# Performance work log

Hardware: AMD Instinct MI355X
Metric: run time of the kernel (lower is better)

The kernel has to match this reference:

```python
import jax, jax.numpy as jnp
import numpy as np
from jax import lax

V = 30000   # vocab (input_types)
D = 512     # model_dim
H = D // 2  # per-direction LSTM hidden
R = 64      # relation_types
B = 32      # batch
T = 512     # seq len
E = 64      # max entities
L = 2       # lstm layers


def setup_inputs() -> dict:
    key = jax.random.key(0)
    ks = jax.random.split(key, 12)
    s = 0.02
    sents = jax.random.randint(ks[0], (B, T), 0, V, dtype=jnp.int64)
    # ent_inds[b, k] = (ent_id, start, end); -1 sentinel marks padding
    ids = np.tile(np.arange(E), (B, 1))
    starts = ids * 8
    ends = starts + 4  # 4-token spans, max end = 63*8+4 = 508 <= T
    ent = np.stack([ids, starts, ends], axis=-1).astype(np.int64)
    for b in range(1, B, 2):
        ent[b, E - 8:] = -1  # ragged: odd batches have 56 entities
    ent_inds = jnp.asarray(ent)
    emb = jax.random.normal(ks[1], (V, D), jnp.float32) * s
    Wih = jax.random.normal(ks[2], (L, 2, 4 * H, D), jnp.float32) * s
    Whh = jax.random.normal(ks[3], (L, 2, 4 * H, H), jnp.float32) * s
    bih = jnp.zeros((L, 2, 4 * H), jnp.float32)
    bhh = jnp.zeros((L, 2, 4 * H), jnp.float32)
    ln_g = jnp.ones((D,), jnp.float32)
    ln_b = jnp.zeros((D,), jnp.float32)
    rel1_w = jax.random.normal(ks[4], (D, D), jnp.float32) * s
    rel1_b = jnp.zeros((D,), jnp.float32)
    rel2_w = jax.random.normal(ks[5], (D, D), jnp.float32) * s
    rel2_b = jnp.zeros((D,), jnp.float32)
    proj_w = jax.random.normal(ks[6], (D, D), jnp.float32) * s
    proj_b = jnp.zeros((D,), jnp.float32)
    dec_w = jax.random.normal(ks[7], (R, D), jnp.float32) * s
    dec_b = jnp.zeros((R,), jnp.float32)
    return dict(sents=sents, ent_inds=ent_inds, max_ents=E, emb=emb,
                Wih=Wih, Whh=Whh, bih=bih, bhh=bhh, ln_g=ln_g, ln_b=ln_b,
                rel1_w=rel1_w, rel1_b=rel1_b, rel2_w=rel2_w, rel2_b=rel2_b,
                proj_w=proj_w, proj_b=proj_b, dec_w=dec_w, dec_b=dec_b)


def _lstm_dir(x, Wih, Whh, bih, bhh, reverse):
    # x: [B, T, Din] -> [B, T, H]; PyTorch gate order i, f, g, o
    xs = jnp.swapaxes(x, 0, 1)  # [T, B, Din]
    bsz = xs.shape[1]
    h0 = jnp.zeros((bsz, Whh.shape[1]), x.dtype)
    c0 = jnp.zeros_like(h0)

    def step(carry, xt):
        h, c = carry
        z = xt @ Wih.T + h @ Whh.T + bih + bhh
        i, f, g, o = jnp.split(z, 4, axis=-1)
        c = jax.nn.sigmoid(f) * c + jax.nn.sigmoid(i) * jnp.tanh(g)
        h = jax.nn.sigmoid(o) * jnp.tanh(c)
        return (h, c), h

    _, ys = lax.scan(step, (h0, c0), xs, reverse=reverse)
    return jnp.swapaxes(ys, 0, 1)


def _bilstm(x, Wih, Whh, bih, bhh):
    for l in range(L):
        fwd = _lstm_dir(x, Wih[l, 0], Whh[l, 0], bih[l, 0], bhh[l, 0], False)
        bwd = _lstm_dir(x, Wih[l, 1], Whh[l, 1], bih[l, 1], bhh[l, 1], True)
        x = jnp.concatenate([fwd, bwd], axis=-1)
    return x


def _forward(sents, ent_inds, max_ents, emb, Wih, Whh, bih, bhh, ln_g, ln_b,
             rel1_w, rel1_b, rel2_w, rel2_b, proj_w, proj_b, dec_w, dec_b):
    x = emb[sents]                                   # [B,T,D]
    x = _bilstm(x, Wih, Whh, bih, bhh)               # [B,T,D]
    bs, _, hd = x.shape
    # ragged span mean-pool via inclusive prefix sums
    csum = jnp.concatenate([jnp.zeros((bs, 1, hd), x.dtype),
                            jnp.cumsum(x, axis=1)], axis=1)  # [B,T+1,D]
    ids, st, en = ent_inds[..., 0], ent_inds[..., 1], ent_inds[..., 2]
    valid = ids >= 0                                 # [B,E]
    sid = jnp.where(valid, ids, 0)
    sst = jnp.where(valid, st, 0)
    sen = jnp.where(valid, en, 1)
    b_idx = jnp.arange(bs)[:, None]
    seg_sum = csum[b_idx, sen] - csum[b_idx, sst]    # [B,E,D]
    length = jnp.maximum(sen - sst, 1).astype(x.dtype)
    means = jnp.where(valid[..., None], seg_sum / length[..., None], 0.0)
    cont = jnp.zeros((bs, max_ents, hd), x.dtype).at[b_idx, sid].add(means)
    mask = jnp.zeros((bs, max_ents), x.dtype).at[b_idx, sid].add(
        valid.astype(x.dtype))
    mask = jnp.clip(mask, 0.0, 1.0)
    # LayerNorm
    mu = jnp.mean(cont, axis=-1, keepdims=True)
    var = jnp.var(cont, axis=-1, keepdims=True)
    cw = (cont - mu) / jnp.sqrt(var + 1e-5) * ln_g + ln_b
    rel1 = cw @ rel1_w.T + rel1_b                    # [B,E,D]
    rel2 = cw @ rel2_w.T + rel2_b                    # [B,E,D]
    out = jax.nn.relu(rel1[:, None, :, :] + rel2[:, :, None, :])  # [B,E,E,D]
    out = jax.nn.relu(out @ proj_w.T + proj_b)
    out = out @ dec_w.T + dec_b                      # [B,E,E,R]
    out = out * mask[:, :, None, None] * mask[:, None, :, None]
    return jax.nn.log_softmax(out, axis=-1)


def reference(sents, ent_inds, max_ents, emb, Wih, Whh, bih, bhh, ln_g, ln_b,
              rel1_w, rel1_b, rel2_w, rel2_b, proj_w, proj_b, dec_w, dec_b):
    return _forward(sents, ent_inds, max_ents, emb, Wih, Whh, bih, bhh,
                    ln_g, ln_b, rel1_w, rel1_b, rel2_w, rel2_b,
                    proj_w, proj_b, dec_w, dec_b)
```

## Files before the change

### kernel.cpp

```cpp
#include <hip/hip_runtime.h>

typedef unsigned short u16;
typedef unsigned int u32;

#define Bsz 32
#define Tlen 512
#define Dm 512
#define Hh 256
#define G4 1024
#define Ee 64
#define Rr 64
#define BT 16384
#define BE 2048

using bshort8 = __attribute__((ext_vector_type(8))) short;
using f32x16  = __attribute__((ext_vector_type(16))) float;
using i32x4   = __attribute__((ext_vector_type(4))) int;
#define MFMA32(a, b, c) __builtin_amdgcn_mfma_f32_32x32x16_bf16(a, b, c, 0, 0, 0)
#define MFMAI8(a, b, c) __builtin_amdgcn_mfma_i32_16x16x64_i8(a, b, c, 0, 0, 0)

__device__ __forceinline__ float b2f(u16 v) {
    union { u32 u; float f; } x; x.u = ((u32)v) << 16; return x.f;
}
__device__ __forceinline__ u16 f2b(float f) {
    union { float f; u32 u; } x; x.f = f;
    u32 r = (x.u + 0x7fffu + ((x.u >> 16) & 1u)) >> 16;
    return (u16)r;
}
__device__ __forceinline__ u32 pk2(float a, float b) {
    return (u32)f2b(a) | ((u32)f2b(b) << 16);
}
__device__ __forceinline__ bool is_bf16_mode(const u32* flagp) {
    return *flagp == 0x3F803F80u;
}
__device__ __forceinline__ float fsig(float x) {
    return __builtin_amdgcn_rcpf(1.f + __expf(-x));
}
__device__ __forceinline__ float ftanh(float x) {
    return 1.f - 2.f * __builtin_amdgcn_rcpf(1.f + __expf(2.f * x));
}
__device__ __forceinline__ float hsc_from(int bits) {
    float p = __int_as_float(bits);
    return p > 0.f ? fminf(2.f * p, 1.f) : 1.f;
}
__device__ __forceinline__ void sync_lds_only() {
    asm volatile("s_waitcnt lgkmcnt(0)" ::: "memory");
    __builtin_amdgcn_s_barrier();
}

struct Ptr10 { const void* p[10]; };
__global__ __launch_bounds__(256) void cvt_fused(Ptr10 srcs, float* __restrict__ dst,
        const u32* __restrict__ flagp) {
    bool bf = is_bf16_mode(flagp);
    int i = blockIdx.x * 256 + threadIdx.x;
    if (i >= 535104) return;
    const int off[10] = {0, 4096, 8192, 8704, 9216, 271360,
                         271872, 534016, 534528, 535040};
    int seg = 0;
#pragma unroll
    for (int k = 1; k < 10; ++k) seg += (i >= off[k]) ? 1 : 0;
    int local = i - off[seg];
    const void* s = srcs.p[seg];
    dst[i] = bf ? b2f(((const u16*)s)[local]) : ((const float*)s)[local];
}

__global__ __launch_bounds__(256) void cvtb_any(const void* __restrict__ src,
        u16* __restrict__ dst, int n, const u32* __restrict__ flagp) {
    bool bf = is_bf16_mode(flagp);
    int i = blockIdx.x * 256 + threadIdx.x;
    if (i >= n) return;
    dst[i] = bf ? ((const u16*)src)[i] : f2b(((const float*)src)[i]);
}

__global__ __launch_bounds__(256) void cvtb4_kernel(const float* __restrict__ src,
        u16* __restrict__ dst, int n4) {
    int i = blockIdx.x * 256 + threadIdx.x;
    if (i >= n4) return;
    float4 v = ((const float4*)src)[i];
    ushort4 o;
    o.x = f2b(v.x); o.y = f2b(v.y); o.z = f2b(v.z); o.w = f2b(v.w);
    ((ushort4*)dst)[i] = o;
}

__global__ __launch_bounds__(256) void whh_quant(const void* __restrict__ whh,
        signed char* __restrict__ qw, float* __restrict__ wsc,
        const u32* __restrict__ flagp) {
    bool bf = is_bf16_mode(flagp);
    int row = blockIdx.x * 4 + (threadIdx.x >> 6);
    int l = threadIdx.x & 63;
    long base = (long)row * 256 + l * 4;
    float v0, v1, v2, v3;
    if (bf) {
        ushort4 uv = *(const ushort4*)((const u16*)whh + base);
        v0 = b2f(uv.x); v1 = b2f(uv.y); v2 = b2f(uv.z); v3 = b2f(uv.w);
    } else {
        float4 fv = *(const float4*)((const float*)whh + base);
        v0 = fv.x; v1 = fv.y; v2 = fv.z; v3 = fv.w;
    }
    float m = fmaxf(fmaxf(fabsf(v0), fabsf(v1)), fmaxf(fabsf(v2), fabsf(v3)));
#pragma unroll
    for (int mk = 32; mk > 0; mk >>= 1) m = fmaxf(m, __shfl_xor(m, mk));
    float inv = m > 0.f ? 127.f / m : 0.f;
    int q0 = (int)rintf(fminf(fmaxf(v0 * inv, -127.f), 127.f));
    int q1 = (int)rintf(fminf(fmaxf(v1 * inv, -127.f), 127.f));
    int q2 = (int)rintf(fminf(fmaxf(v2 * inv, -127.f), 127.f));
    int q3 = (int)rintf(fminf(fmaxf(v3 * inv, -127.f), 127.f));
    u32 pk = (u32)(q0 & 255) | ((u32)(q1 & 255) << 8) |
             ((u32)(q2 & 255) << 16) | ((u32)(q3 & 255) << 24);
    ((u32*)qw)[row * 64 + l] = pk;
    if (l == 0) wsc[row] = m * (1.f / 127.f);
}

__global__ __launch_bounds__(256) void embed_kernel(const int* __restrict__ sents,
        const void* __restrict__ emb, float* __restrict__ x, const u32* __restrict__ flagp) {
    bool bf = is_bf16_mode(flagp);
    int i = blockIdx.x * 256 + threadIdx.x;
    int tok = i >> 7, c4 = (i & 127) * 4;
    long base = (long)sents[tok] * Dm + c4;
    float4 o;
    if (bf) {
        ushort4 uv = *(const ushort4*)((const u16*)emb + base);
        o = make_float4(b2f(uv.x), b2f(uv.y), b2f(uv.z), b2f(uv.w));
    } else {
        o = *(const float4*)((const float*)emb + base);
    }
    *(float4*)(x + (long)tok * Dm + c4) = o;
}

__global__ __launch_bounds__(256) void gemm_nt(const float* __restrict__ A,
        const float* __restrict__ W, const float* __restrict__ b1, const float* __restrict__ b2,
        float* __restrict__ C, int M, int N, int K,
        long wStride, long bStride, long cStride) {
    __shared__ float As[16][132];
    __shared__ float Ws[16][132];
    int z = blockIdx.z;
    const float* Wz = W + (long)z * wStride;
    float* Cz = C + (long)z * cStride;
    int m0 = blockIdx.y * 128, n0 = blockIdx.x * 128;
    int t = threadIdx.x, ty = t >> 4, tx = t & 15;

    float bias[8];
#pragma unroll
    for (int j = 0; j < 8; ++j) {
        int n = n0 + tx * 8 + j;
        float bb = 0.f;
        if (b1) bb += b1[z * bStride + n];
        if (b2) bb += b2[z * bStride + n];
        bias[j] = bb;
    }
    float acc[8][8] = {};
    int lrow = t >> 2, lkq = (t & 3) * 4;
    for (int k0 = 0; k0 < K; k0 += 16) {
        __syncthreads();
#pragma unroll
        for (int h = 0; h < 2; ++h) {
            int row = lrow + h * 64;
            float4 av = *(const float4*)&A[(long)(m0 + row) * K + k0 + lkq];
            As[lkq + 0][row] = av.x; As[lkq + 1][row] = av.y;
            As[lkq + 2][row] = av.z; As[lkq + 3][row] = av.w;
            float4 wv = *(const float4*)&Wz[(long)(n0 + row) * K + k0 + lkq];
            Ws[lkq + 0][row] = wv.x; Ws[lkq + 1][row] = wv.y;
            Ws[lkq + 2][row] = wv.z; Ws[lkq + 3][row] = wv.w;
        }
        __syncthreads();
#pragma unroll
        for (int k = 0; k < 16; ++k) {
            float4 a0 = *(const float4*)&As[k][ty * 8];
            float4 a1 = *(const float4*)&As[k][ty * 8 + 4];
            float4 w0 = *(const float4*)&Ws[k][tx * 8];
            float4 w1 = *(const float4*)&Ws[k][tx * 8 + 4];
            float av8[8] = {a0.x,a0.y,a0.z,a0.w,a1.x,a1.y,a1.z,a1.w};
            float wv8[8] = {w0.x,w0.y,w0.z,w0.w,w1.x,w1.y,w1.z,w1.w};
#pragma unroll
            for (int i = 0; i < 8; ++i)
#pragma unroll
                for (int j = 0; j < 8; ++j)
                    acc[i][j] += av8[i] * wv8[j];
        }
    }
#pragma unroll
    for (int i = 0; i < 8; ++i) {
        long m = m0 + ty * 8 + i;
#pragma unroll
        for (int jq = 0; jq < 2; ++jq) {
            int n = n0 + tx * 8 + jq * 4;
            float4 o;
            o.x = acc[i][jq*4+0] + bias[jq*4+0];
            o.y = acc[i][jq*4+1] + bias[jq*4+1];
            o.z = acc[i][jq*4+2] + bias[jq*4+2];
            o.w = acc[i][jq*4+3] + bias[jq*4+3];
            *(float4*)&Cz[m * N + n] = o;
        }
    }
}

__global__ __launch_bounds__(256, 2) void gemm_mfma(const u16* __restrict__ A,
        const u16* __restrict__ W, const float* __restrict__ b1, const float* __restrict__ b2,
        float* __restrict__ C, int M, int N, int K,
        long wStride, long bStride, long cStride) {
    __shared__ u16 As[4 * 128 * 8];
    __shared__ u16 Bs[4 * 128 * 8];
    int z = blockIdx.z;
    const u16* Wz = W + (long)z * wStride;
    float* Cz = C + (long)z * cStride;
    int m0 = blockIdx.y * 128, n0 = blockIdx.x * 128;
    int t = threadIdx.x;
    int w = t >> 6, l = t & 63, ln31 = l & 31, lk = l >> 5;
    int mh = (w >> 1) * 64, nh = (w & 1) * 64;
    f32x16 acc[2][2];
#pragma unroll
    for (int i = 0; i < 2; ++i)
#pragma unroll
        for (int j = 0; j < 2; ++j)
#pragma unroll
            for (int r = 0; r < 16; ++r) acc[i][j][r] = 0.f;

    int srow = t >> 1, skb = (t & 1) * 2;
    const u16* Arow = A + (long)(m0 + srow) * K + skb * 8;
    const u16* Wrow = Wz + (long)(n0 + srow) * K + skb * 8;
    for (int k0 = 0; k0 < K; k0 += 32) {
        __syncthreads();
        uint4 a0 = *(const uint4*)(Arow + k0);
        uint4 a1 = *(const uint4*)(Arow + k0 + 8);
        uint4 b0 = *(const uint4*)(Wrow + k0);
        uint4 b1v = *(const uint4*)(Wrow + k0 + 8);
        *(uint4*)(As + ((skb * 128 + srow) << 3)) = a0;
        *(uint4*)(As + (((skb + 1) * 128 + srow) << 3)) = a1;
        *(uint4*)(Bs + ((skb * 128 + srow) << 3)) = b0;
        *(uint4*)(Bs + (((skb + 1) * 128 + srow) << 3)) = b1v;
        __syncthreads();
#pragma unroll
        for (int ks = 0; ks < 2; ++ks) {
            int kb = ks * 2 + lk;
            bshort8 av0 = *(const bshort8*)(As + ((kb * 128 + mh + ln31) << 3));
            bshort8 av1 = *(const bshort8*)(As + ((kb * 128 + mh + 32 + ln31) << 3));
            bshort8 bv0 = *(const bshort8*)(Bs + ((kb * 128 + nh + ln31) << 3));
            bshort8 bv1 = *(const bshort8*)(Bs + ((kb * 128 + nh + 32 + ln31) << 3));
            acc[0][0] = MFMA32(av0, bv0, acc[0][0]);
            acc[0][1] = MFMA32(av0, bv1, acc[0][1]);
            acc[1][0] = MFMA32(av1, bv0, acc[1][0]);
            acc[1][1] = MFMA32(av1, bv1, acc[1][1]);
        }
    }
#pragma unroll
    for (int j = 0; j < 2; ++j) {
        int n = n0 + nh + j * 32 + ln31;
        float bb = 0.f;
        if (b1) bb += b1[z * bStride + n];
        if (b2) bb += b2[z * bStride + n];
#pragma unroll
        for (int i = 0; i < 2; ++i) {
            long mb = m0 + mh + i * 32 + 4 * lk;
#pragma unroll
            for (int r = 0; r < 16; ++r) {
                long mrow = mb + (r & 3) + 8 * (r >> 2);
                Cz[mrow * N + n] = acc[i][j][r] + bb;
            }
        }
    }
}

__global__ __attribute__((amdgpu_flat_work_group_size(512, 512)))
__attribute__((amdgpu_waves_per_eu(1, 2)))
void lstm_scan_i8(
        const float* __restrict__ xp, const signed char* __restrict__ qw,
        const float* __restrict__ wsc, float* __restrict__ y) {
    __shared__ u32 h8[2][64];
    __shared__ int hmx[4];
    int bid = blockIdx.x;
    int dir = bid & 1, b = bid >> 1;
    int t = threadIdx.x, w = t >> 6, l = t & 63;
    int ln15 = l & 15, lk4 = l >> 4;
    int e8 = ln15 & 7;
    int u = w * 32 + lk4 * 8 + e8;
    bool wr = (ln15 < 8);

    i32x4 wf[8][4];
    {
        int q = ln15 >> 2, j = ln15 & 3;
        const signed char* rp = qw + ((long)dir << 18)
            + ((long)(j * 256 + w * 32 + q * 8) << 8) + lk4 * 16;
#pragma unroll
        for (int e = 0; e < 8; ++e)
#pragma unroll
            for (int ks = 0; ks < 4; ++ks)
                wf[e][ks] = *(const i32x4*)(rp + ((long)e << 8) + ks * 64);
    }
    float scg0, scg1, scg2, scg3;
    {
        const float* wl = wsc + (dir << 10);
        scg0 = wl[u]       * (1.f / 127.f);
        scg1 = wl[256 + u] * (1.f / 127.f);
        scg2 = wl[512 + u] * (1.f / 127.f);
        scg3 = wl[768 + u] * (1.f / 127.f);
    }
    const float* xpb = xp + (long)dir * BT * G4 + ((long)b << 19);
    float c = 0.f, am = 0.f;
    float xq0, xq1, xq2, xq3;
    {
        int tt0 = dir ? 511 : 0;
        const float* xr = xpb + ((long)tt0 << 10) + u;
        xq0 = xr[0]; xq1 = xr[256]; xq2 = xr[512]; xq3 = xr[768];
    }
    if (t < 64) h8[0][t] = 0u;
    if (t < 4) hmx[t] = 0;
    __syncthreads();

#pragma unroll 1
    for (int s = 0; s < Tlen; ++s) {
        int tt = dir ? (511 - s) : s;
        int p = s & 1;
        float hrec  = hsc_from(hmx[(s + 3) & 3]);
        float usedq = hsc_from(hmx[s & 3]);
        i32x4 bv0 = *(const i32x4*)((const char*)h8[p] + 0 * 64 + lk4 * 16);
        i32x4 bv1 = *(const i32x4*)((const char*)h8[p] + 1 * 64 + lk4 * 16);
        i32x4 bv2 = *(const i32x4*)((const char*)h8[p] + 2 * 64 + lk4 * 16);
        i32x4 bv3 = *(const i32x4*)((const char*)h8[p] + 3 * 64 + lk4 * 16);
        float nx0 = 0.f, nx1 = 0.f, nx2 = 0.f, nx3 = 0.f;
        if (s < 511) {
            int tn = dir ? (510 - s) : (s + 1);
            const float* xr = xpb + ((long)tn << 10) + u;
            nx0 = xr[0]; nx1 = xr[256]; nx2 = xr[512]; nx3 = xr[768];
        }
        i32x4 acc[8];
#pragma unroll
        for (int e = 0; e < 8; ++e) {
            acc[e][0] = 0; acc[e][1] = 0; acc[e][2] = 0; acc[e][3] = 0;
        }
#pragma unroll
        for (int e = 0; e < 8; ++e) {
            acc[e] = MFMAI8(wf[e][0], bv0, acc[e]);
            acc[e] = MFMAI8(wf[e][1], bv1, acc[e]);
            acc[e] = MFMAI8(wf[e][2], bv2, acc[e]);
            acc[e] = MFMAI8(wf[e][3], bv3, acc[e]);
        }
        {
            float amr = fmaxf(am, __shfl_xor(am, 32));
            amr = fmaxf(amr, __shfl_xor(amr, 16));
            amr = fmaxf(amr, __shfl_xor(amr, 4));
            amr = fmaxf(amr, __shfl_xor(amr, 2));
            amr = fmaxf(amr, __shfl_xor(amr, 1));
            if (l == 0) atomicMax(&hmx[(s + 1) & 3], __float_as_int(amr));
            if (t == 0) hmx[(s + 2) & 3] = 0;
        }
        i32x4 t0 = (e8 & 1) ? acc[1] : acc[0];
        i32x4 t1 = (e8 & 1) ? acc[3] : acc[2];
        i32x4 t2 = (e8 & 1) ? acc[5] : acc[4];
        i32x4 t3 = (e8 & 1) ? acc[7] : acc[6];
        i32x4 u0 = (e8 & 2) ? t1 : t0;
        i32x4 u1 = (e8 & 2) ? t3 : t2;
        i32x4 zv = (e8 & 4) ? u1 : u0;
        float zi = (float)zv[0] * (scg0 * hrec) + xq0;
        float zf = (float)zv[1] * (scg1 * hrec) + xq1;
        float zg = (float)zv[2] * (scg2 * hrec) + xq2;
        float zo = (float)zv[3] * (scg3 * hrec) + xq3;
        c = fsig(zf) * c + fsig(zi) * ftanh(zg);
        float h = fsig(zo) * ftanh(c);
        if (wr)
            y[(((long)((b << 9) + tt)) << 9) + (dir << 8) + u] = h;
        int qi = (int)rintf(fminf(fmaxf(h * (127.f / usedq), -127.f), 127.f));
        if (wr)
            ((signed char*)h8[p ^ 1])[u] = (signed char)qi;
        am = fabsf(h);
        xq0 = nx0; xq1 = nx1; xq2 = nx2; xq3 = nx3;
        sync_lds_only();
    }
}

__global__ __launch_bounds__(128) void pool_kernel(const float* __restrict__ y,
        const int* __restrict__ ent, float* __restrict__ cont, float* __restrict__ mask) {
    int be = blockIdx.x, b = be >> 6;
    int id = ent[be * 3], st = ent[be * 3 + 1], en = ent[be * 3 + 2];
    if (id < 0 || id >= Ee) return;
    int len = en - st; if (len < 1) len = 1;
    float inv = 1.f / (float)len;
    int t = threadIdx.x;
    for (int d = t; d < Dm; d += 128) {
        float s = 0.f;
        for (int q = st; q < en; ++q) s += y[((long)b * Tlen + q) * Dm + d];
        atomicAdd(&cont[((long)b * Ee + id) * Dm + d], s * inv);
    }
    if (t == 0) atomicAdd(&mask[b * Ee + id], 1.f);
}

__global__ __launch_bounds__(256) void ln_kernel(const float* __restrict__ cont,
        const float* __restrict__ g, const float* __restrict__ bta, float* __restrict__ cw) {
    __shared__ float red[256];
    int be = blockIdx.x, t = threadIdx.x;
    const float* xr = cont + (long)be * Dm;
    float v0 = xr[t], v1 = xr[t + 256];
    red[t] = v0 + v1;
    __syncthreads();
#pragma unroll
    for (int o = 128; o > 0; o >>= 1) {
        if (t < o) red[t] += red[t + o];
        __syncthreads();
    }
    float mu = red[0] * (1.f / 512.f);
    __syncthreads();
    float d0 = v0 - mu, d1 = v1 - mu;
    red[t] = d0 * d0 + d1 * d1;
    __syncthreads();
#pragma unroll
    for (int o = 128; o > 0; o >>= 1) {
        if (t < o) red[t] += red[t + o];
        __syncthreads();
    }
    float rs = rsqrtf(red[0] * (1.f / 512.f) + 1e-5f);
    cw[(long)be * Dm + t]       = d0 * rs * g[t] + bta[t];
    cw[(long)be * Dm + t + 256] = d1 * rs * g[t + 256] + bta[t + 256];
}

__global__ __launch_bounds__(256, 2) void pair_head_mfma(
        const float* __restrict__ r1o, const float* __restrict__ r2o,
        const u16* __restrict__ pwB, const float* __restrict__ proj_b,
        const u16* __restrict__ dwB, const float* __restrict__ dec_b,
        const float* __restrict__ mask, void* __restrict__ outv,
        const u32* __restrict__ flagp) {
    __shared__ u16 Ub[64 * 64 * 8];
    __shared__ float red[256];
    float* lg = (float*)Ub;
    int bid = blockIdx.x, b = bid >> 6;
    int t = threadIdx.x;
    int w = t >> 6, l = t & 63, ln31 = l & 31, lk = l >> 5;
    bool bf = is_bf16_mode(flagp);

    {
        int m = t & 63, kseg = t >> 6;
        const float* r1r = r1o + ((long)b * Ee + m) * Dm + kseg * 128;
        const float* r2r = r2o + (long)bid * Dm + kseg * 128;
#pragma unroll
        for (int q = 0; q < 16; ++q) {
            float4 x0 = *(const float4*)(r1r + q * 8);
            float4 x1 = *(const float4*)(r1r + q * 8 + 4);
            float4 y0 = *(const float4*)(r2r + q * 8);
            float4 y1 = *(const float4*)(r2r + q * 8 + 4);
            uint4 o;
            o.x = pk2(fmaxf(x0.x + y0.x, 0.f), fmaxf(x0.y + y0.y, 0.f));
            o.y = pk2(fmaxf(x0.z + y0.z, 0.f), fmaxf(x0.w + y0.w, 0.f));
            o.z = pk2(fmaxf(x1.x + y1.x, 0.f), fmaxf(x1.y + y1.y, 0.f));
            o.w = pk2(fmaxf(x1.z + y1.z, 0.f), fmaxf(x1.w + y1.w, 0.f));
            int kb = kseg * 16 + q;
            *(uint4*)(Ub + (((kb << 6) + m) << 3)) = o;
        }
    }
    __syncthreads();

    f32x16 acc[2][4];
#pragma unroll
    for (int i = 0; i < 2; ++i)
#pragma unroll
        for (int j = 0; j < 4; ++j)
#pragma unroll
            for (int r = 0; r < 16; ++r) acc[i][j][r] = 0.f;
    const u16* pwW = pwB + (long)(w * 128) * Dm;
#pragma unroll 1
    for (int ks = 0; ks < 32; ++ks) {
        int kb = ks * 2 + lk;
        bshort8 a0 = *(const bshort8*)(Ub + (((kb << 6) + ln31) << 3));
        bshort8 a1 = *(const bshort8*)(Ub + (((kb << 6) + 32 + ln31) << 3));
#pragma unroll
        for (int nt = 0; nt < 4; ++nt) {
            bshort8 bv = *(const bshort8*)(pwW + (long)(nt * 32 + ln31) * Dm
                                           + ks * 16 + lk * 8);
            acc[0][nt] = MFMA32(a0, bv, acc[0][nt]);
            acc[1][nt] = MFMA32(a1, bv, acc[1][nt]);
        }
    }
    __syncthreads();

#pragma unroll
    for (int nt = 0; nt < 4; ++nt) {
        int n = w * 128 + nt * 32 + ln31;
        float pb = proj_b[n];
        int kbp = n >> 3, ni = n & 7;
#pragma unroll
        for (int i = 0; i < 2; ++i) {
#pragma unroll
            for (int r = 0; r < 16; ++r) {
                int m = i * 32 + (r & 3) + 8 * (r >> 2) + 4 * lk;
                Ub[(((kbp << 6) + m) << 3) + ni] = f2b(fmaxf(acc[i][nt][r] + pb, 0.f));
            }
        }
    }
    __syncthreads();

    f32x16 acc2;
#pragma unroll
    for (int r = 0; r < 16; ++r) acc2[r] = 0.f;
    int mt = w >> 1, nt2 = w & 1;
#pragma unroll 1
    for (int ks = 0; ks < 32; ++ks) {
        int kb = ks * 2 + lk;
        bshort8 a = *(const bshort8*)(Ub + (((kb << 6) + mt * 32 + ln31) << 3));
        bshort8 bv = *(const bshort8*)(dwB + (long)(nt2 * 32 + ln31) * Dm
                                       + ks * 16 + lk * 8);
        acc2 = MFMA32(a, bv, acc2);
    }
    __syncthreads();

    float mx = fminf(mask[bid], 1.f);
    {
        int r = nt2 * 32 + ln31;
        float db = dec_b[r];
#pragma unroll
        for (int rg = 0; rg < 16; ++rg) {
            int yy = mt * 32 + (rg & 3) + 8 * (rg >> 2) + 4 * lk;
            float my = fminf(mask[b * Ee + yy], 1.f);
            lg[yy * 68 + r] = (acc2[rg] + db) * mx * my;
        }
    }
    __syncthreads();

    {
        int yy = t >> 2, part = t & 3;
        float m = -1e30f;
#pragma unroll
        for (int q = 0; q < 16; ++q) m = fmaxf(m, lg[yy * 68 + part * 16 + q]);
        red[t] = m;
        __syncthreads();
        float m4 = fmaxf(fmaxf(red[yy * 4], red[yy * 4 + 1]),
                         fmaxf(red[yy * 4 + 2], red[yy * 4 + 3]));
        __syncthreads();
        float ssum = 0.f;
#pragma unroll
        for (int q = 0; q < 16; ++q) ssum += expf(lg[yy * 68 + part * 16 + q] - m4);
        red[t] = ssum;
        __syncthreads();
        float lse = m4 + logf(red[yy * 4] + red[yy * 4 + 1] + red[yy * 4 + 2] + red[yy * 4 + 3]);
        long obase = ((long)bid * 64 + yy) * 64;
        if (bf) {
            u16* o16 = (u16*)outv;
#pragma unroll
            for (int q = 0; q < 16; ++q)
                o16[obase + part * 16 + q] = f2b(lg[yy * 68 + part * 16 + q] - lse);
        } else {
            float* o32 = (float*)outv;
#pragma unroll
            for (int q = 0; q < 16; ++q)
                o32[obase + part * 16 + q] = lg[yy * 68 + part * 16 + q] - lse;
        }
    }
}

extern "C" void kernel_launch(void* const* d_in, const int* in_sizes, int n_in,
                              void* d_out, int out_size, void* d_ws, size_t ws_size,
                              hipStream_t stream) {
    (void)in_sizes; (void)n_in; (void)out_size; (void)ws_size;
    const int* sents = (const int*)d_in[0];
    const int* ent   = (const int*)d_in[1];
    const void* emb  = d_in[3];
    const void* Wih  = d_in[4];
    const void* Whh  = d_in[5];
    const void* bih  = d_in[6];
    const void* bhh  = d_in[7];
    const u32* flagp = (const u32*)d_in[8];

    float* ws = (float*)d_ws;
    float* bufA = ws;
    float* bufB = bufA + (long)BT * Dm;
    float* xp   = bufB + (long)BT * Dm;
    float* fWhh = xp + 2L * BT * G4;
    float* cont = fWhh + 4L * G4 * Hh;
    float* maskp= cont + (long)BE * Dm;
    float* cw   = maskp + BE;
    float* r1   = cw + (long)BE * Dm;
    float* r2   = r1 + (long)BE * Dm;
    float* fbih = r2 + (long)BE * Dm;
    float* fbhh = fbih + 4L * G4;
    float* flng = fbhh + 4L * G4;
    float* flnb = flng + Dm;
    float* fr1w = flnb + Dm;
    float* fr1b = fr1w + (long)Dm * Dm;
    float* fr2w = fr1b + Dm;
    float* fr2b = fr2w + (long)Dm * Dm;
    float* fpb  = fr2b + Dm;
    float* fdb  = fpb + Dm;
    u16* wihB = (u16*)(fdb + Rr);
    u16* pwB  = wihB + 4L * G4 * Dm;
    u16* dwB  = pwB + (long)Dm * Dm;

    signed char* qwhh = (signed char*)fWhh;
    float* wscA = (float*)(qwhh + (4L * G4 * Hh));
    u16* xb = (u16*)cont;

    Ptr10 ps;
    ps.p[0] = bih;      ps.p[1] = bhh;      ps.p[2] = d_in[8];  ps.p[3] = d_in[9];
    ps.p[4] = d_in[10]; ps.p[5] = d_in[11]; ps.p[6] = d_in[12]; ps.p[7] = d_in[13];
    ps.p[8] = d_in[15]; ps.p[9] = d_in[17];
    cvt_fused<<<(535104 + 255) / 256, 256, 0, stream>>>(ps, fbih, flagp);
    whh_quant<<<1024, 256, 0, stream>>>(Whh, qwhh, wscA, flagp);
    cvtb_any<<<(4 * G4 * Dm) / 256, 256, 0, stream>>>(Wih, wihB, 4 * G4 * Dm, flagp);
    cvtb_any<<<(Dm * Dm) / 256, 256, 0, stream>>>(d_in[14], pwB, Dm * Dm, flagp);
    cvtb_any<<<(Rr * Dm) / 256, 256, 0, stream>>>(d_in[16], dwB, Rr * Dm, flagp);

    embed_kernel<<<(BT * Dm / 4) / 256, 256, 0, stream>>>(sents, emb, bufA, flagp);

    float* lin = bufA; float* lout = bufB;
    for (int l = 0; l < 2; ++l) {
        cvtb4_kernel<<<(BT * Dm / 4) / 256, 256, 0, stream>>>(lin, xb, BT * Dm / 4);
        gemm_mfma<<<dim3(G4 / 128, BT / 128, 2), 256, 0, stream>>>(
            xb, wihB + (long)l * 2 * G4 * Dm, fbih + l * 2 * G4, fbhh + l * 2 * G4,
            xp, BT, G4, Dm, (long)G4 * Dm, (long)G4, (long)BT * G4);
        lstm_scan_i8<<<64, 512, 0, stream>>>(xp, qwhh + (long)l * 2 * G4 * Hh,
                                             wscA + l * 2 * G4, lout);
        float* tmp = lin; lin = lout; lout = tmp;
    }
    hipMemsetAsync(cont, 0, ((long)BE * Dm + BE) * sizeof(float), stream);
    pool_kernel<<<BE, 128, 0, stream>>>(lin, ent, cont, maskp);
    ln_kernel<<<BE, 256, 0, stream>>>(cont, flng, flnb, cw);
    gemm_nt<<<dim3(Dm / 128, BE / 128, 1), 256, 0, stream>>>(cw, fr1w, fr1b, nullptr,
            r1, BE, Dm, Dm, 0, 0, 0);
    gemm_nt<<<dim3(Dm / 128, BE / 128, 1), 256, 0, stream>>>(cw, fr2w, fr2b, nullptr,
            r2, BE, Dm, Dm, 0, 0, 0);
    pair_head_mfma<<<BE, 256, 0, stream>>>(r1, r2, pwB, fpb, dwB, fdb, maskp,
                                           d_out, flagp);
}
```

Baseline: 1.828 ms.

## Batch four sequences per LSTM scan block to fill MFMA columns

The int8 LSTM recurrence kernel now processes four batch elements per workgroup, using the 16 MFMA columns for four batches instead of padding them. Each block uses 1024 threads, each lane owns one hidden unit for one batch, and only 16 blocks launch instead of 64. The aim is to stop wasting MFMA lanes and to halve the per-lane weight fragments and select logic. In exchange, each CU now does more serial work per step, which lowers parallelism across the GPU and raises the cost of each block barrier.

```diff
diff --git a/kernel.cpp b/kernel.cpp
--- a/kernel.cpp
+++ b/kernel.cpp
@@ -260,28 +260,27 @@
     }
 }
 
-__global__ __attribute__((amdgpu_flat_work_group_size(512, 512)))
-__attribute__((amdgpu_waves_per_eu(1, 2)))
+__global__ __attribute__((amdgpu_flat_work_group_size(1024, 1024)))
+__attribute__((amdgpu_waves_per_eu(4, 4)))
 void lstm_scan_i8(
         const float* __restrict__ xp, const signed char* __restrict__ qw,
         const float* __restrict__ wsc, float* __restrict__ y) {
-    __shared__ u32 h8[2][64];
-    __shared__ int hmx[4];
+    __shared__ u32 h8[2][4][68];
+    __shared__ int hmx[4][4];
     int bid = blockIdx.x;
-    int dir = bid & 1, b = bid >> 1;
+    int dir = bid & 1, bq = bid >> 1;
     int t = threadIdx.x, w = t >> 6, l = t & 63;
     int ln15 = l & 15, lk4 = l >> 4;
-    int e8 = ln15 & 7;
-    int u = w * 32 + lk4 * 8 + e8;
-    bool wr = (ln15 < 8);
-
-    i32x4 wf[8][4];
+    int bt = ln15 & 3, e2 = ln15 >> 2;
+    int u = w * 16 + lk4 * 4 + e2;
+    int bg = bq * 4 + bt;
+
+    i32x4 wf[4][4];
     {
-        int q = ln15 >> 2, j = ln15 & 3;
         const signed char* rp = qw + ((long)dir << 18)
-            + ((long)(j * 256 + w * 32 + q * 8) << 8) + lk4 * 16;
-#pragma unroll
-        for (int e = 0; e < 8; ++e)
+            + ((long)((ln15 & 3) * 256 + w * 16 + (ln15 >> 2) * 4) << 8) + lk4 * 16;
+#pragma unroll
+        for (int e = 0; e < 4; ++e)
 #pragma unroll
             for (int ks = 0; ks < 4; ++ks)
                 wf[e][ks] = *(const i32x4*)(rp + ((long)e << 8) + ks * 64);
@@ -294,7 +293,7 @@
         scg2 = wl[512 + u] * (1.f / 127.f);
         scg3 = wl[768 + u] * (1.f / 127.f);
     }
-    const float* xpb = xp + (long)dir * BT * G4 + ((long)b << 19);
+    const float* xpb = xp + (long)dir * BT * G4 + ((long)bg << 19);
     float c = 0.f, am = 0.f;
     float xq0, xq1, xq2, xq3;
     {
@@ -302,65 +301,59 @@
         const float* xr = xpb + ((long)tt0 << 10) + u;
         xq0 = xr[0]; xq1 = xr[256]; xq2 = xr[512]; xq3 = xr[768];
     }
-    if (t < 64) h8[0][t] = 0u;
-    if (t < 4) hmx[t] = 0;
+    if (t < 544) ((u32*)h8)[t] = 0u;
+    if (t < 16) hmx[t >> 2][t & 3] = 0;
     __syncthreads();
 
 #pragma unroll 1
     for (int s = 0; s < Tlen; ++s) {
         int tt = dir ? (511 - s) : s;
         int p = s & 1;
-        float hrec  = hsc_from(hmx[(s + 3) & 3]);
-        float usedq = hsc_from(hmx[s & 3]);
-        i32x4 bv0 = *(const i32x4*)((const char*)h8[p] + 0 * 64 + lk4 * 16);
-        i32x4 bv1 = *(const i32x4*)((const char*)h8[p] + 1 * 64 + lk4 * 16);
-        i32x4 bv2 = *(const i32x4*)((const char*)h8[p] + 2 * 64 + lk4 * 16);
-        i32x4 bv3 = *(const i32x4*)((const char*)h8[p] + 3 * 64 + lk4 * 16);
+        float hrec  = hsc_from(hmx[bt][(s + 3) & 3]);
+        float usedq = hsc_from(hmx[bt][s & 3]);
+        const char* hb = (const char*)h8[p][bt];
+        i32x4 bv0 = *(const i32x4*)(hb + 0 * 64 + lk4 * 16);
+        i32x4 bv1 = *(const i32x4*)(hb + 1 * 64 + lk4 * 16);
+        i32x4 bv2 = *(const i32x4*)(hb + 2 * 64 + lk4 * 16);
+        i32x4 bv3 = *(const i32x4*)(hb + 3 * 64 + lk4 * 16);
         float nx0 = 0.f, nx1 = 0.f, nx2 = 0.f, nx3 = 0.f;
         if (s < 511) {
             int tn = dir ? (510 - s) : (s + 1);
             const float* xr = xpb + ((long)tn << 10) + u;
             nx0 = xr[0]; nx1 = xr[256]; nx2 = xr[512]; nx3 = xr[768];
         }
-        i32x4 acc[8];
-#pragma unroll
-        for (int e = 0; e < 8; ++e) {
+        i32x4 acc[4];
+#pragma unroll
+        for (int e = 0; e < 4; ++e) {
             acc[e][0] = 0; acc[e][1] = 0; acc[e][2] = 0; acc[e][3] = 0;
         }
 #pragma unroll
-        for (int e = 0; e < 8; ++e) {
+        for (int e = 0; e < 4; ++e) {
             acc[e] = MFMAI8(wf[e][0], bv0, acc[e]);
             acc[e] = MFMAI8(wf[e][1], bv1, acc[e]);
             acc[e] = MFMAI8(wf[e][2], bv2, acc[e]);
             acc[e] = MFMAI8(wf[e][3], bv3, acc[e]);
         }
         {
-            float amr = fmaxf(am, __shfl_xor(am, 32));
+            float amr = fmaxf(am, __shfl_xor(am, 4));
+            amr = fmaxf(amr, __shfl_xor(amr, 8));
             amr = fmaxf(amr, __shfl_xor(amr, 16));
-            amr = fmaxf(amr, __shfl_xor(amr, 4));
-            amr = fmaxf(amr, __shfl_xor(amr, 2));
-            amr = fmaxf(amr, __shfl_xor(amr, 1));
-            if (l == 0) atomicMax(&hmx[(s + 1) & 3], __float_as_int(amr));
-            if (t == 0) hmx[(s + 2) & 3] = 0;
-        }
-        i32x4 t0 = (e8 & 1) ? acc[1] : acc[0];
-        i32x4 t1 = (e8 & 1) ? acc[3] : acc[2];
-        i32x4 t2 = (e8 & 1) ? acc[5] : acc[4];
-        i32x4 t3 = (e8 & 1) ? acc[7] : acc[6];
-        i32x4 u0 = (e8 & 2) ? t1 : t0;
-        i32x4 u1 = (e8 & 2) ? t3 : t2;
-        i32x4 zv = (e8 & 4) ? u1 : u0;
+            amr = fmaxf(amr, __shfl_xor(amr, 32));
+            if (l < 4) atomicMax(&hmx[l][(s + 1) & 3], __float_as_int(amr));
+            if (t < 4) hmx[t][(s + 2) & 3] = 0;
+        }
+        i32x4 s01 = (e2 & 1) ? acc[1] : acc[0];
+        i32x4 s23 = (e2 & 1) ? acc[3] : acc[2];
+        i32x4 zv  = (e2 & 2) ? s23 : s01;
         float zi = (float)zv[0] * (scg0 * hrec) + xq0;
         float zf = (float)zv[1] * (scg1 * hrec) + xq1;
         float zg = (float)zv[2] * (scg2 * hrec) + xq2;
         float zo = (float)zv[3] * (scg3 * hrec) + xq3;
         c = fsig(zf) * c + fsig(zi) * ftanh(zg);
         float h = fsig(zo) * ftanh(c);
-        if (wr)
-            y[(((long)((b << 9) + tt)) << 9) + (dir << 8) + u] = h;
+        y[(((long)((bg << 9) + tt)) << 9) + (dir << 8) + u] = h;
         int qi = (int)rintf(fminf(fmaxf(h * (127.f / usedq), -127.f), 127.f));
-        if (wr)
-            ((signed char*)h8[p ^ 1])[u] = (signed char)qi;
+        ((signed char*)h8[p ^ 1][bt])[u] = (signed char)qi;
         am = fabsf(h);
         xq0 = nx0; xq1 = nx1; xq2 = nx2; xq3 = nx3;
         sync_lds_only();
@@ -602,8 +595,8 @@
         gemm_mfma<<<dim3(G4 / 128, BT / 128, 2), 256, 0, stream>>>(
             xb, wihB + (long)l * 2 * G4 * Dm, fbih + l * 2 * G4, fbhh + l * 2 * G4,
             xp, BT, G4, Dm, (long)G4 * Dm, (long)G4, (long)BT * G4);
-        lstm_scan_i8<<<64, 512, 0, stream>>>(xp, qwhh + (long)l * 2 * G4 * Hh,
-                                             wscA + l * 2 * G4, lout);
+        lstm_scan_i8<<<16, 1024, 0, stream>>>(xp, qwhh + (long)l * 2 * G4 * Hh,
+                                              wscA + l * 2 * G4, lout);
         float* tmp = lin; lin = lout; lout = tmp;
     }
     hipMemsetAsync(cont, 0, ((long)BE * Dm + BE) * sizeof(float), stream);
```

After: 1.921 ms. 1.05x slower.
